# Optimization experiments

Measured on AMD Instinct MI355X. Metric: run time of the kernel, lower is better.

## Reference

```python
import jax, jax.numpy as jnp
import numpy as np

C = 51  # num_relation


def setup_inputs() -> dict:
    key = jax.random.key(0)
    N_o, N_u, D = 16384, 16384, 1024
    k = jax.random.split(key, 6)
    feat = jax.random.normal(k[0], (N_o + N_u, D), jnp.float32)
    # first N_o rows are labeled (label != 0), remaining N_u rows unlabeled (label == 0)
    label = jnp.concatenate([
        jax.random.randint(k[1], (N_o,), 1, C),
        jnp.zeros((N_u,), jnp.int32),
    ]).astype(jnp.int32)
    W_o = jax.random.normal(k[2], (C, D), jnp.float32) * 0.03
    b_o = jnp.zeros((C,), jnp.float32)
    W = jax.random.normal(k[3], (C, D), jnp.float32) * 0.03
    b = jnp.zeros((C,), jnp.float32)
    cls = jnp.arange(C)
    group_mid_mask = (cls >= 16) & (cls < 36)   # groups[1]
    group_tail_mask = cls >= 36                 # groups[2]
    # runtime torch.randint partner sampling, hoisted to input construction
    idx_m = jax.random.randint(k[4], (2, N_u), 0, N_o)  # 2 mid copies
    idx_t = jax.random.randint(k[5], (3, N_u), 0, N_o)  # 3 tail copies
    return dict(feat=feat, label=label, W_o=W_o, b_o=b_o, W=W, b=b,
                group_mid_mask=group_mid_mask, group_tail_mask=group_tail_mask,
                idx_m=idx_m, idx_t=idx_t)


def reference(feat, label, W_o, b_o, W, b, group_mid_mask, group_tail_mask, idx_m, idx_t):
    n_u = idx_m.shape[1]
    n_o = feat.shape[0] - n_u
    feat_o, feat_u = feat[:n_o], feat[n_o:]
    label_o = label[:n_o]

    # fc_o under no_grad, then softmax / top-1 rank + score
    logits = jax.lax.stop_gradient(feat_u @ W_o.T + b_o)      # [N_u, C]
    p = jax.nn.softmax(logits, axis=1)
    pred = jnp.argmax(p, axis=1)                               # ranks[:,0]
    score = jnp.max(p, axis=1)                                 # score[:,0]

    # group membership + confidence thresholds (heads are unused in the original)
    mid_m = group_mid_mask[pred] & (score > 0.5)
    tail_m = group_tail_mask[pred] & (score > 0.3)

    oh_u = jax.nn.one_hot(pred, C, dtype=feat.dtype)
    oh_o = jax.nn.one_hot(label_o, C, dtype=feat.dtype)

    im = idx_m.reshape(-1)   # [2*N_u]
    it = idx_t.reshape(-1)   # [3*N_u]

    fm = 0.7 * feat_o[im] + 0.3 * jnp.tile(feat_u, (2, 1))
    lm = 0.7 * oh_o[im] + 0.3 * jnp.tile(oh_u, (2, 1))
    ft = 0.7 * feat_o[it] + 0.3 * jnp.tile(feat_u, (3, 1))
    lt = 0.7 * oh_o[it] + 0.3 * jnp.tile(oh_u, (3, 1))

    feat_cat = jnp.concatenate([fm, ft], axis=0)               # [5*N_u, D]
    label_cat = jnp.concatenate([lm, lt], axis=0)              # [5*N_u, C]
    w = jnp.concatenate([jnp.tile(mid_m, 2), jnp.tile(tail_m, 3)]).astype(feat.dtype)

    # soft-label cross entropy on fc(feat_cat); masked mean over selected rows
    logp = jax.nn.log_softmax(feat_cat @ W.T + b, axis=1)
    ce = -(logp * label_cat).sum(axis=1)
    cnt = w.sum()
    return (ce * w).sum() / jnp.maximum(cnt, 1.0)
```

## Files before the change

kernel.cpp:

```cpp
#include <hip/hip_runtime.h>
#include <math.h>

#define DD 1024
#define SN 52
#define NU 16384
#define NO 16384
#define CEBLK 5120

typedef short short8 __attribute__((ext_vector_type(8)));
typedef float f32x4 __attribute__((ext_vector_type(4)));

__device__ __forceinline__ unsigned short f2b(float x) {
    unsigned int u = __float_as_uint(x);
    u += 0x7FFFu + ((u >> 16) & 1u);
    return (unsigned short)(u >> 16);
}

__device__ __forceinline__ short8 cvt8(float4 a, float4 b) {
    short8 r;
    r[0] = (short)f2b(a.x); r[1] = (short)f2b(a.y);
    r[2] = (short)f2b(a.z); r[3] = (short)f2b(a.w);
    r[4] = (short)f2b(b.x); r[5] = (short)f2b(b.y);
    r[6] = (short)f2b(b.z); r[7] = (short)f2b(b.w);
    return r;
}

__global__ __launch_bounds__(256) void convW(const float* __restrict__ W,
                                             const float* __restrict__ W_o,
                                             unsigned short* __restrict__ Wcat) {
    const int n = blockIdx.x;
    const int k = threadIdx.x * 4;
    const float* src = nullptr;
    if (n < 64) { if (n < 51) src = W + (size_t)n * DD; }
    else        { if (n - 64 < 51) src = W_o + (size_t)(n - 64) * DD; }
    float4 v = src ? *(const float4*)(src + k) : make_float4(0.f, 0.f, 0.f, 0.f);
    ushort4 o;
    o.x = f2b(v.x); o.y = f2b(v.y); o.z = f2b(v.z); o.w = f2b(v.w);
    *(ushort4*)(Wcat + (size_t)n * DD + k) = o;
}

__device__ __forceinline__ void stage_tile(const float* __restrict__ feat,
                                           float* __restrict__ buf,
                                           int m0, int k0, int w, int lane) {
#pragma unroll
    for (int i = 0; i < 4; ++i) {
        const int r = (i * 4 + w) * 4 + (lane >> 4);
        const int p = lane & 15;
        const int g = p ^ (r & 7);
        const float* gp = feat + (size_t)(m0 + r) * DD + k0 + g * 4;
        __builtin_amdgcn_global_load_lds(
            (const __attribute__((address_space(1))) void*)gp,
            (__attribute__((address_space(3))) void*)(buf + (i * 4 + w) * 256),
            16, 0, 0);
    }
}

template <int NFR>
__device__ __forceinline__ void gemm_wave(const float* __restrict__ feat,
                                          const unsigned short* __restrict__ Wcat,
                                          const float* __restrict__ b_o,
                                          int m0, float* __restrict__ Bmat,
                                          int* __restrict__ flags,
                                          float* __restrict__ As) {
    const int tid = threadIdx.x;
    const int lane = tid & 63;
    const int w = tid >> 6;
    const int m = lane & 15;
    const int quad = lane >> 4;
    const int s = m & 7;
    const unsigned short* bp = Wcat + (size_t)m * DD + quad * 8;

    f32x4 acc[NFR];
#pragma unroll
    for (int nf = 0; nf < NFR; ++nf) acc[nf] = (f32x4){0.f, 0.f, 0.f, 0.f};

    stage_tile(feat, As, m0, 0, w, lane);

    for (int kt = 0; kt < 16; ++kt) {
        float* buf = As + (kt & 1) * 4096;
        __syncthreads();
        if (kt < 15)
            stage_tile(feat, As + ((kt + 1) & 1) * 4096, m0, (kt + 1) * 64, w, lane);
        short8 breg[2][NFR];
#pragma unroll
        for (int h = 0; h < 2; ++h)
#pragma unroll
            for (int nf = 0; nf < NFR; ++nf)
                breg[h][nf] = *(const short8*)(bp + (size_t)nf * 16 * DD + kt * 64 + h * 32);
        const float* arow = buf + (w * 16 + m) * 64;
#pragma unroll
        for (int h = 0; h < 2; ++h) {
            const int c0 = h * 8 + 2 * quad;
            const float4 f0 = *(const float4*)(arow + ((c0) ^ s) * 4);
            const float4 f1 = *(const float4*)(arow + ((c0 + 1) ^ s) * 4);
            const short8 af = cvt8(f0, f1);
#pragma unroll
            for (int nf = 0; nf < NFR; ++nf)
                acc[nf] = __builtin_amdgcn_mfma_f32_16x16x32_bf16(af, breg[h][nf], acc[nf], 0, 0, 0);
        }
    }

    const int rbase = m0 + w * 16 + quad * 4;
#pragma unroll
    for (int nf = 0; nf < 4; ++nf) {
        const int colL = nf * 16 + m;
        if (colL < 51) {
#pragma unroll
            for (int r = 0; r < 4; ++r)
                Bmat[(size_t)(rbase + r) * SN + colL] = acc[nf][r];
        }
    }
    if constexpr (NFR == 8) {
        float boc[4];
#pragma unroll
        for (int c = 0; c < 4; ++c) {
            const int col = c * 16 + m;
            boc[c] = (col < 51) ? b_o[col] : 0.f;
        }
#pragma unroll
        for (int r = 0; r < 4; ++r) {
            float z[4];
            float mx = acc[4][r] + boc[0];
            int mi = m;
            z[0] = mx;
#pragma unroll
            for (int c = 1; c < 4; ++c) {
                const int col = c * 16 + m;
                z[c] = (col < 51) ? acc[4 + c][r] + boc[c] : -INFINITY;
                if (z[c] > mx) { mx = z[c]; mi = col; }
            }
#pragma unroll
            for (int off = 1; off < 16; off <<= 1) {
                const float om = __shfl_xor(mx, off);
                const int oi = __shfl_xor(mi, off);
                if (om > mx || (om == mx && oi < mi)) { mx = om; mi = oi; }
            }
            float e = 0.f;
#pragma unroll
            for (int c = 0; c < 4; ++c)
                if (c * 16 + m < 51) e += expf(z[c] - mx);
#pragma unroll
            for (int off = 1; off < 16; off <<= 1) e += __shfl_xor(e, off);
            const float score = 1.f / e;
            const int mid = (mi >= 16 && mi < 36 && score > 0.5f) ? 1 : 0;
            const int tail = (mi >= 36 && score > 0.3f) ? 1 : 0;
            if (m == 0) flags[rbase + r - NO] = mi | (mid << 8) | (tail << 9);
        }
    }
}

__global__ __launch_bounds__(256) void gemm_mfma(const float* __restrict__ feat,
                                                 const unsigned short* __restrict__ Wcat,
                                                 const float* __restrict__ b_o,
                                                 float* __restrict__ Bmat,
                                                 int* __restrict__ flags) {
    __shared__ float As[2 * 64 * 64];
    const int m0 = blockIdx.x * 64;
    if (m0 < NO) gemm_wave<4>(feat, Wcat, b_o, m0, Bmat, flags, As);
    else         gemm_wave<8>(feat, Wcat, b_o, m0, Bmat, flags, As);
}

__global__ __launch_bounds__(256) void cekernel(const float* __restrict__ B,
                                                const float* __restrict__ bb,
                                                const int* __restrict__ label,
                                                const int* __restrict__ idxm,
                                                const int* __restrict__ idxt,
                                                const int* __restrict__ flags,
                                                double* __restrict__ pnum,
                                                int* __restrict__ pcnt) {
    __shared__ float snum[4];
    __shared__ int scnt[4];
    const int w = threadIdx.x >> 6;
    const int lane = threadIdx.x & 63;
    float csum = 0.f;
    int ccnt = 0;
#pragma unroll
    for (int it = 0; it < 4; ++it) {
        const int j = (blockIdx.x * 4 + w) * 4 + it;
        int u, o, active;
        if (j < 2 * NU) {
            u = j & (NU - 1);
            o = idxm[j];
            active = (flags[u] >> 8) & 1;
        } else {
            const int j2 = j - 2 * NU;
            u = j2 & (NU - 1);
            o = idxt[j2];
            active = (flags[u] >> 9) & 1;
        }
        if (active) {
            const float* Bo = B + (size_t)o * SN;
            const float* Bu = B + (size_t)(NO + u) * SN;
            float z = -INFINITY;
            if (lane < 51) z = 0.7f * Bo[lane] + 0.3f * Bu[lane] + bb[lane];
            float m = z;
#pragma unroll
            for (int off = 1; off < 64; off <<= 1) m = fmaxf(m, __shfl_xor(m, off));
            float e = (lane < 51) ? expf(z - m) : 0.f;
#pragma unroll
            for (int off = 1; off < 64; off <<= 1) e += __shfl_xor(e, off);
            const float lse = m + logf(e);
            const int lo = label[o];
            const int pu = flags[u] & 255;
            const float zlo = __shfl(z, lo);
            const float zpu = __shfl(z, pu);
            csum += lse - 0.7f * zlo - 0.3f * zpu;
            ccnt += 1;
        }
    }
    if (lane == 0) { snum[w] = csum; scnt[w] = ccnt; }
    __syncthreads();
    if (threadIdx.x == 0) {
        pnum[blockIdx.x] = (double)snum[0] + (double)snum[1] +
                           (double)snum[2] + (double)snum[3];
        pcnt[blockIdx.x] = scnt[0] + scnt[1] + scnt[2] + scnt[3];
    }
}

__global__ __launch_bounds__(256) void finalize(const double* __restrict__ pnum,
                                                const int* __restrict__ pcnt,
                                                float* __restrict__ out) {
    __shared__ double sd[4];
    __shared__ int sc[4];
    const int w = threadIdx.x >> 6;
    const int lane = threadIdx.x & 63;
    double s = 0.0;
    int c = 0;
    for (int i = threadIdx.x; i < CEBLK; i += 256) {
        s += pnum[i];
        c += pcnt[i];
    }
#pragma unroll
    for (int off = 1; off < 64; off <<= 1) {
        s += __shfl_xor(s, off);
        c += __shfl_xor(c, off);
    }
    if (lane == 0) { sd[w] = s; sc[w] = c; }
    __syncthreads();
    if (threadIdx.x == 0) {
        const double n = sd[0] + sd[1] + sd[2] + sd[3];
        const int cc = sc[0] + sc[1] + sc[2] + sc[3];
        out[0] = (float)(n / (cc > 1 ? (double)cc : 1.0));
    }
}

extern "C" void kernel_launch(void* const* d_in, const int* in_sizes, int n_in,
                              void* d_out, int out_size, void* d_ws, size_t ws_size,
                              hipStream_t stream) {
    const float* feat = (const float*)d_in[0];
    const int* label = (const int*)d_in[1];
    const float* W_o = (const float*)d_in[2];
    const float* b_o = (const float*)d_in[3];
    const float* W = (const float*)d_in[4];
    const float* b = (const float*)d_in[5];
    const int* idxm = (const int*)d_in[8];
    const int* idxt = (const int*)d_in[9];

    char* ws = (char*)d_ws;
    float* Bmat = (float*)ws;
    double* pnum = (double*)(ws + 6815744);
    int* pcnt = (int*)(ws + 6815744 + 40960);
    int* flags = (int*)(ws + 6815744 + 40960 + 20480);
    unsigned short* Wcat =
        (unsigned short*)(ws + 6815744 + 40960 + 20480 + 65536);

    convW<<<128, 256, 0, stream>>>(W, W_o, Wcat);
    gemm_mfma<<<(NO + NU) / 64, 256, 0, stream>>>(feat, Wcat, b_o, Bmat, flags);
    cekernel<<<CEBLK, 256, 0, stream>>>(Bmat, b, label, idxm, idxt, flags, pnum, pcnt);
    finalize<<<1, 256, 0, stream>>>(pnum, pcnt, (float*)d_out);
}
```

Measured before the change: 241.7 us.

## Stage weights in LDS with 3-stage async pipeline and split unlabeled GEMM tiles

Rewrites the projection GEMM so the bf16 weight tiles are also loaded into LDS via async global-to-LDS copies, rather than read directly from global memory by each wave. A triple-buffered K pipeline with 32-wide K steps uses explicit vmcnt waits, so the prefetch runs two steps ahead. Unlabeled rows now use 32-row tiles with waves split across the two weight matrices, which gives 768 blocks with balanced per-block work. The cost is more LDS (36KB), more barriers per K step, and reliance on hand-counted vmcnt values.

```diff
diff --git a/kernel.cpp b/kernel.cpp
--- a/kernel.cpp
+++ b/kernel.cpp
@@ -23,6 +23,12 @@
     r[4] = (short)f2b(b.x); r[5] = (short)f2b(b.y);
     r[6] = (short)f2b(b.z); r[7] = (short)f2b(b.w);
     return r;
+}
+
+__device__ __forceinline__ void gl_lds(const void* g, void* l) {
+    __builtin_amdgcn_global_load_lds(
+        (const __attribute__((address_space(1))) void*)g,
+        (__attribute__((address_space(3))) void*)l, 16, 0, 0);
 }
 
 __global__ __launch_bounds__(256) void convW(const float* __restrict__ W,
@@ -39,125 +45,163 @@
     *(ushort4*)(Wcat + (size_t)n * DD + k) = o;
 }
 
-__device__ __forceinline__ void stage_tile(const float* __restrict__ feat,
-                                           float* __restrict__ buf,
-                                           int m0, int k0, int w, int lane) {
-#pragma unroll
-    for (int i = 0; i < 4; ++i) {
-        const int r = (i * 4 + w) * 4 + (lane >> 4);
-        const int p = lane & 15;
-        const int g = p ^ (r & 7);
-        const float* gp = feat + (size_t)(m0 + r) * DD + k0 + g * 4;
-        __builtin_amdgcn_global_load_lds(
-            (const __attribute__((address_space(1))) void*)gp,
-            (__attribute__((address_space(3))) void*)(buf + (i * 4 + w) * 256),
-            16, 0, 0);
-    }
-}
-
-template <int NFR>
-__device__ __forceinline__ void gemm_wave(const float* __restrict__ feat,
+template <int IS_U>
+__device__ __forceinline__ void gemm_body(const float* __restrict__ feat,
                                           const unsigned short* __restrict__ Wcat,
                                           const float* __restrict__ b_o,
                                           int m0, float* __restrict__ Bmat,
-                                          int* __restrict__ flags,
-                                          float* __restrict__ As) {
+                                          int* __restrict__ flags, char* lds) {
     const int tid = threadIdx.x;
     const int lane = tid & 63;
     const int w = tid >> 6;
     const int m = lane & 15;
     const int quad = lane >> 4;
     const int s = m & 7;
-    const unsigned short* bp = Wcat + (size_t)m * DD + quad * 8;
-
-    f32x4 acc[NFR];
-#pragma unroll
-    for (int nf = 0; nf < NFR; ++nf) acc[nf] = (f32x4){0.f, 0.f, 0.f, 0.f};
-
-    stage_tile(feat, As, m0, 0, w, lane);
-
-    for (int kt = 0; kt < 16; ++kt) {
-        float* buf = As + (kt & 1) * 4096;
-        __syncthreads();
-        if (kt < 15)
-            stage_tile(feat, As + ((kt + 1) & 1) * 4096, m0, (kt + 1) * 64, w, lane);
-        short8 breg[2][NFR];
-#pragma unroll
-        for (int h = 0; h < 2; ++h)
-#pragma unroll
-            for (int nf = 0; nf < NFR; ++nf)
-                breg[h][nf] = *(const short8*)(bp + (size_t)nf * 16 * DD + kt * 64 + h * 32);
-        const float* arow = buf + (w * 16 + m) * 64;
-#pragma unroll
-        for (int h = 0; h < 2; ++h) {
-            const int c0 = h * 8 + 2 * quad;
-            const float4 f0 = *(const float4*)(arow + ((c0) ^ s) * 4);
-            const float4 f1 = *(const float4*)(arow + ((c0 + 1) ^ s) * 4);
-            const short8 af = cvt8(f0, f1);
-#pragma unroll
-            for (int nf = 0; nf < NFR; ++nf)
-                acc[nf] = __builtin_amdgcn_mfma_f32_16x16x32_bf16(af, breg[h][nf], acc[nf], 0, 0, 0);
-        }
-    }
-
-    const int rbase = m0 + w * 16 + quad * 4;
-#pragma unroll
-    for (int nf = 0; nf < 4; ++nf) {
-        const int colL = nf * 16 + m;
-        if (colL < 51) {
-#pragma unroll
-            for (int r = 0; r < 4; ++r)
-                Bmat[(size_t)(rbase + r) * SN + colL] = acc[nf][r];
-        }
-    }
-    if constexpr (NFR == 8) {
-        float boc[4];
-#pragma unroll
-        for (int c = 0; c < 4; ++c) {
-            const int col = c * 16 + m;
-            boc[c] = (col < 51) ? b_o[col] : 0.f;
-        }
-#pragma unroll
-        for (int r = 0; r < 4; ++r) {
-            float z[4];
-            float mx = acc[4][r] + boc[0];
-            int mi = m;
-            z[0] = mx;
-#pragma unroll
-            for (int c = 1; c < 4; ++c) {
+    const int s2 = m & 3;
+
+    const char *gs0, *gs1, *gs2;
+    int lo0, lo1, lo2, st1;
+    if constexpr (!IS_U) {
+        { const int r = w * 16 + (lane >> 3);
+          const int g = (lane & 7) ^ (r & 7);
+          gs0 = (const char*)(feat + (size_t)(m0 + r) * DD + g * 4); lo0 = (w * 2) * 1024; }
+        { const int r = w * 16 + 8 + (lane >> 3);
+          const int g = (lane & 7) ^ (r & 7);
+          gs1 = (const char*)(feat + (size_t)(m0 + r) * DD + g * 4); lo1 = (w * 2 + 1) * 1024; }
+        { const int r = w * 16 + (lane >> 2);
+          const int g = (lane & 3) ^ (r & 3);
+          gs2 = (const char*)(Wcat + (size_t)r * DD + g * 8); lo2 = 8192 + w * 1024; }
+        st1 = 128;
+    } else {
+        { const int r = w * 8 + (lane >> 3);
+          const int g = (lane & 7) ^ (r & 7);
+          gs0 = (const char*)(feat + (size_t)(NO + m0 + r) * DD + g * 4); lo0 = w * 1024; }
+        { const int r = (w * 2) * 16 + (lane >> 2);
+          const int g = (lane & 3) ^ (r & 3);
+          gs1 = (const char*)(Wcat + (size_t)r * DD + g * 8); lo1 = 4096 + (w * 2) * 1024; }
+        { const int r = (w * 2 + 1) * 16 + (lane >> 2);
+          const int g = (lane & 3) ^ (r & 3);
+          gs2 = (const char*)(Wcat + (size_t)r * DD + g * 8); lo2 = 4096 + (w * 2 + 1) * 1024; }
+        st1 = 64;
+    }
+
+    f32x4 acc[4];
+#pragma unroll
+    for (int nf = 0; nf < 4; ++nf) acc[nf] = (f32x4){0.f, 0.f, 0.f, 0.f};
+
+    const int rA = (IS_U ? (w & 1) * 16 : w * 16) + m;
+    const int rBbase = (IS_U ? (w >> 1) * 64 : 0) + m;
+    const int Bofs = IS_U ? 4096 : 8192;
+
+#define STAGE(t, buf)                                  \
+    do {                                               \
+        gl_lds(gs0 + (size_t)(t) * 128, (buf) + lo0);  \
+        gl_lds(gs1 + (size_t)(t) * st1, (buf) + lo1);  \
+        gl_lds(gs2 + (size_t)(t) * 64,  (buf) + lo2);  \
+    } while (0)
+
+    STAGE(0, lds);
+    STAGE(1, lds + 12288);
+
+    int bc = 0;
+    for (int kt = 0; kt < 32; ++kt) {
+        if (kt < 30) {
+            const int bi2 = (bc == 0) ? 2 : bc - 1;
+            STAGE(kt + 2, lds + bi2 * 12288);
+            asm volatile("s_waitcnt vmcnt(6)\n\ts_barrier" ::: "memory");
+        } else if (kt == 30) {
+            asm volatile("s_waitcnt vmcnt(3)\n\ts_barrier" ::: "memory");
+        } else {
+            asm volatile("s_waitcnt vmcnt(0)\n\ts_barrier" ::: "memory");
+        }
+        const char* buf = lds + bc * 12288;
+        const float4 f0 = *(const float4*)(buf + rA * 128 + ((2 * quad) ^ s) * 16);
+        const float4 f1 = *(const float4*)(buf + rA * 128 + ((2 * quad + 1) ^ s) * 16);
+        const short8 af = cvt8(f0, f1);
+#pragma unroll
+        for (int nf = 0; nf < 4; ++nf) {
+            const short8 bf =
+                *(const short8*)(buf + Bofs + (rBbase + nf * 16) * 64 + (quad ^ s2) * 16);
+            acc[nf] = __builtin_amdgcn_mfma_f32_16x16x32_bf16(af, bf, acc[nf], 0, 0, 0);
+        }
+        bc = (bc == 2) ? 0 : bc + 1;
+    }
+#undef STAGE
+
+    if constexpr (!IS_U) {
+        const int rbase = m0 + w * 16 + quad * 4;
+#pragma unroll
+        for (int nf = 0; nf < 4; ++nf) {
+            const int col = nf * 16 + m;
+            if (col < 51) {
+#pragma unroll
+                for (int r = 0; r < 4; ++r)
+                    Bmat[(size_t)(rbase + r) * SN + col] = acc[nf][r];
+            }
+        }
+    } else {
+        const int wm = w & 1, wn = w >> 1;
+        const int rloc = m0 + wm * 16 + quad * 4;
+        if (wn == 0) {
+#pragma unroll
+            for (int nf = 0; nf < 4; ++nf) {
+                const int col = nf * 16 + m;
+                if (col < 51) {
+#pragma unroll
+                    for (int r = 0; r < 4; ++r)
+                        Bmat[(size_t)(NO + rloc + r) * SN + col] = acc[nf][r];
+                }
+            }
+        } else {
+            float boc[4];
+#pragma unroll
+            for (int c = 0; c < 4; ++c) {
                 const int col = c * 16 + m;
-                z[c] = (col < 51) ? acc[4 + c][r] + boc[c] : -INFINITY;
-                if (z[c] > mx) { mx = z[c]; mi = col; }
+                boc[c] = (col < 51) ? b_o[col] : 0.f;
             }
 #pragma unroll
-            for (int off = 1; off < 16; off <<= 1) {
-                const float om = __shfl_xor(mx, off);
-                const int oi = __shfl_xor(mi, off);
-                if (om > mx || (om == mx && oi < mi)) { mx = om; mi = oi; }
+            for (int r = 0; r < 4; ++r) {
+                float z[4];
+                float mx = acc[0][r] + boc[0];
+                int mi = m;
+                z[0] = mx;
+#pragma unroll
+                for (int c = 1; c < 4; ++c) {
+                    const int col = c * 16 + m;
+                    z[c] = (col < 51) ? acc[c][r] + boc[c] : -INFINITY;
+                    if (z[c] > mx) { mx = z[c]; mi = col; }
+                }
+#pragma unroll
+                for (int off = 1; off < 16; off <<= 1) {
+                    const float om = __shfl_xor(mx, off);
+                    const int oi = __shfl_xor(mi, off);
+                    if (om > mx || (om == mx && oi < mi)) { mx = om; mi = oi; }
+                }
+                float e = 0.f;
+#pragma unroll
+                for (int c = 0; c < 4; ++c)
+                    if (c * 16 + m < 51) e += expf(z[c] - mx);
+#pragma unroll
+                for (int off = 1; off < 16; off <<= 1) e += __shfl_xor(e, off);
+                const float score = 1.f / e;
+                const int mid = (mi >= 16 && mi < 36 && score > 0.5f) ? 1 : 0;
+                const int tail = (mi >= 36 && score > 0.3f) ? 1 : 0;
+                if (m == 0) flags[rloc + r] = mi | (mid << 8) | (tail << 9);
             }
-            float e = 0.f;
-#pragma unroll
-            for (int c = 0; c < 4; ++c)
-                if (c * 16 + m < 51) e += expf(z[c] - mx);
-#pragma unroll
-            for (int off = 1; off < 16; off <<= 1) e += __shfl_xor(e, off);
-            const float score = 1.f / e;
-            const int mid = (mi >= 16 && mi < 36 && score > 0.5f) ? 1 : 0;
-            const int tail = (mi >= 36 && score > 0.3f) ? 1 : 0;
-            if (m == 0) flags[rbase + r - NO] = mi | (mid << 8) | (tail << 9);
-        }
-    }
-}
-
-__global__ __launch_bounds__(256) void gemm_mfma(const float* __restrict__ feat,
-                                                 const unsigned short* __restrict__ Wcat,
-                                                 const float* __restrict__ b_o,
-                                                 float* __restrict__ Bmat,
-                                                 int* __restrict__ flags) {
-    __shared__ float As[2 * 64 * 64];
-    const int m0 = blockIdx.x * 64;
-    if (m0 < NO) gemm_wave<4>(feat, Wcat, b_o, m0, Bmat, flags, As);
-    else         gemm_wave<8>(feat, Wcat, b_o, m0, Bmat, flags, As);
+        }
+    }
+}
+
+__global__ __launch_bounds__(256, 4) void gemm_mfma(const float* __restrict__ feat,
+                                                    const unsigned short* __restrict__ Wcat,
+                                                    const float* __restrict__ b_o,
+                                                    float* __restrict__ Bmat,
+                                                    int* __restrict__ flags) {
+    __shared__ __attribute__((aligned(16))) char lds[3 * 12288];
+    if (blockIdx.x < 256)
+        gemm_body<0>(feat, Wcat, b_o, blockIdx.x * 64, Bmat, flags, lds);
+    else
+        gemm_body<1>(feat, Wcat, b_o, (blockIdx.x - 256) * 32, Bmat, flags, lds);
 }
 
 __global__ __launch_bounds__(256) void cekernel(const float* __restrict__ B,
@@ -265,7 +309,7 @@
         (unsigned short*)(ws + 6815744 + 40960 + 20480 + 65536);
 
     convW<<<128, 256, 0, stream>>>(W, W_o, Wcat);
-    gemm_mfma<<<(NO + NU) / 64, 256, 0, stream>>>(feat, Wcat, b_o, Bmat, flags);
+    gemm_mfma<<<768, 256, 0, stream>>>(feat, Wcat, b_o, Bmat, flags);
     cekernel<<<CEBLK, 256, 0, stream>>>(Bmat, b, label, idxm, idxt, flags, pnum, pcnt);
     finalize<<<1, 256, 0, stream>>>(pnum, pcnt, (float*)d_out);
 }
```

Result: faster. 234.4 us (-3.0%).
